# Kernel tuning notes

Hardware: AMD Instinct MI355X
Metric: run time of the kernel (lower is better)

## Reference

```python
import jax, jax.numpy as jnp
import numpy as np

KERNEL_NUM = 21
SIGMA = 0.1
EXACT_SIGMA = 0.001

def _kernel_params():
    mus, sigmas = [], []
    for i in range(KERNEL_NUM):
        mu = 1.0 / (KERNEL_NUM - 1) + 2.0 * i / (KERNEL_NUM - 1) - 1.0
        sigma = SIGMA
        if mu > 1.0:
            sigma = EXACT_SIGMA
            mu = 1.0
        mus.append(mu)
        sigmas.append(sigma)
    return np.asarray(mus, np.float32), np.asarray(sigmas, np.float32)

MU, SIG = _kernel_params()  # [K], [K]

def setup_inputs() -> dict:
    key = jax.random.key(0)
    k = jax.random.split(key, 8)
    V, D, B, L, R = 50000, 128, 512, 30, 200
    emb = jax.random.normal(k[0], (V, D), dtype=jnp.float32)
    W = jax.random.normal(k[1], (1, KERNEL_NUM), dtype=jnp.float32) * 0.1
    b = jax.random.normal(k[2], (1,), dtype=jnp.float32) * 0.1
    query1 = jax.random.randint(k[3], (B, L), 0, V, dtype=jnp.int32)
    doc1 = jax.random.randint(k[4], (B, R), 0, V, dtype=jnp.int32)
    query2 = jax.random.randint(k[5], (B, L), 0, V, dtype=jnp.int32)
    doc2 = jax.random.randint(k[6], (B, R), 0, V, dtype=jnp.int32)
    return {"emb": emb, "W": W, "b": b, "query1": query1, "doc1": doc1,
            "query2": query2, "doc2": doc2}

def _l2norm(x):
    # F.normalize(p=2, dim=-1): x / max(||x||, eps)
    n = jnp.sqrt(jnp.sum(x * x, axis=-1, keepdims=True))
    return x / jnp.maximum(n, 1e-12)

def _predict(emb, W, b, q, d):
    eq = _l2norm(emb[q])              # [B,L,D]
    ed = _l2norm(emb[d])              # [B,R,D]
    M = jnp.einsum('bld,brd->blr', eq, ed)  # matching matrix [B,L,R]
    # multi-Gaussian kernel bank: [B,L,R,K]
    Kmat = jnp.exp(-0.5 * (M[..., None] - MU) ** 2 / (SIG ** 2))
    km = jnp.sum(jnp.log1p(jnp.sum(Kmat, axis=2)), axis=1)  # [B,K]
    return km @ W.T + b               # [B,1]

def reference(emb, W, b, query1, doc1, query2, doc2):
    logits1 = _predict(emb, W, b, query1, doc1)
    logits2 = _predict(emb, W, b, query2, doc2)
    return jax.nn.sigmoid(logits1 - logits2)
```

## Files before the change

### kernel.cpp

```cpp
#include <hip/hip_runtime.h>
#include <hip/hip_fp16.h>
#include <math.h>

#define V   50000
#define DIM 128
#define BB  512
#define LQ  30
#define RD  200
#define KN  21

typedef __attribute__((ext_vector_type(8))) _Float16 f16x8;
typedef __attribute__((ext_vector_type(4))) float f32x4;
typedef __attribute__((ext_vector_type(2))) float f32x2;

#if __has_builtin(__builtin_amdgcn_exp2f)
#define EXP2F(x) __builtin_amdgcn_exp2f(x)
#else
#define EXP2F(x) __expf((x) * 0.69314718f)
#endif

#define ALPHA 72.1347520f
#define E10   22026.4657948f

static __device__ __forceinline__ f16x8 as_hfrag(int4 v) {
    return __builtin_bit_cast(f16x8, v);
}
static __device__ __forceinline__ unsigned pk2h(float a, float b) {
    return __builtin_bit_cast(unsigned, __builtin_amdgcn_cvt_pkrtz(a, b));
}
static __device__ __forceinline__ unsigned hscale(unsigned u, __half2 s) {
    return __builtin_bit_cast(unsigned, __hmul2(__builtin_bit_cast(__half2, u), s));
}

static __device__ __forceinline__ void gather_row_f16(const float* __restrict__ rowp,
                                                      int g, int4* f) {
    float ss = 0.0f;
#pragma unroll
    for (int ks = 0; ks < 4; ++ks) {
        const float4* p = reinterpret_cast<const float4*>(rowp + ks * 32 + g * 8);
        float4 a = p[0], b = p[1];
        ss = fmaf(a.x, a.x, fmaf(a.y, a.y, fmaf(a.z, a.z, fmaf(a.w, a.w, ss))));
        ss = fmaf(b.x, b.x, fmaf(b.y, b.y, fmaf(b.z, b.z, fmaf(b.w, b.w, ss))));
        f[ks].x = (int)pk2h(a.x, a.y);
        f[ks].y = (int)pk2h(a.z, a.w);
        f[ks].z = (int)pk2h(b.x, b.y);
        f[ks].w = (int)pk2h(b.z, b.w);
    }
    ss += __shfl_xor(ss, 16);
    ss += __shfl_xor(ss, 32);
    const float inv = rsqrtf(fmaxf(ss, 1e-24f));
    const __half2 h2 = __float2half2_rn(inv);
#pragma unroll
    for (int ks = 0; ks < 4; ++ks) {
        f[ks].x = (int)hscale((unsigned)f[ks].x, h2);
        f[ks].y = (int)hscale((unsigned)f[ks].y, h2);
        f[ks].z = (int)hscale((unsigned)f[ks].z, h2);
        f[ks].w = (int)hscale((unsigned)f[ks].w, h2);
    }
}

static __device__ __forceinline__ void bank4_pk(f32x4 pv, int4 dt, int qt,
                                                f32x2* ks2, float& cnt) {
    const float mv[4] = {pv[0], pv[1], pv[2], pv[3]};
    const int   dv[4] = {dt.x, dt.y, dt.z, dt.w};
    f32x2 t[4], u[4];
#pragma unroll
    for (int i = 0; i < 4; ++i) {
        float m  = mv[i];
        float dA = m + 0.5f, dB = m - 0.5f;
        float tA = EXP2F(-ALPHA * dA * (dA + 0.9f));
        float tB = EXP2F(-ALPHA * dB * (dB + 0.9f));
        float uB = EXP2F(14.4269504f * dB);
        float uA = uB * E10;
        t[i] = f32x2{tA, tB};
        u[i] = f32x2{uA, uB};
        cnt += (dv[i] == qt) ? 1.0f : 0.0f;
    }
#pragma unroll
    for (int k = 0; k < 10; ++k) {
        ks2[k] += (t[0] + t[1]) + (t[2] + t[3]);
        t[0] *= u[0]; t[1] *= u[1]; t[2] *= u[2]; t[3] *= u[3];
    }
}

__global__ __launch_bounds__(256, 4) void knrm_main(
    const float* __restrict__ emb, const float* __restrict__ W,
    const int* __restrict__ q1, const int* __restrict__ d1,
    const int* __restrict__ q2, const int* __restrict__ d2,
    float* __restrict__ logits)
{
    __shared__ int sQtok[32];
    __shared__ __align__(16) int sDtok[256];
    __shared__ float kred[4][32][KN];

    const int pb = blockIdx.x;
    const int pair = pb >> 9, b = pb & 511;
    const int* qind = (pair ? q2 : q1) + b * LQ;
    const int* dind = (pair ? d2 : d1) + b * RD;

    const int tid = threadIdx.x;
    const int lane = tid & 63, w = tid >> 6;
    const int r = lane & 15, g = lane >> 4;

    if (tid < 32) sQtok[tid] = (tid < LQ) ? qind[tid] : -2;
    { int c = tid; sDtok[c] = (c < RD) ? dind[c] : -1; }

    const int qiA = qind[r];
    const int qiB = qind[(16 + r) < LQ ? (16 + r) : LQ - 1];
    int4 qa[4], qb[4];
    gather_row_f16(emb + (size_t)qiA * DIM, g, qa);
    gather_row_f16(emb + (size_t)qiB * DIM, g, qb);

    __syncthreads();

    const int qt0 = sQtok[r], qt1 = sQtok[16 + r];
    const int4* sDtok4 = (const int4*)sDtok;

    f32x2 ks0[10], ks1[10];
#pragma unroll
    for (int k = 0; k < 10; ++k) { ks0[k] = f32x2{0.f, 0.f}; ks1[k] = f32x2{0.f, 0.f}; }
    float cnt0 = 0.0f, cnt1 = 0.0f;

    const int ns = (w < 3) ? 4 : 1;
#pragma unroll 2
    for (int s = 0; s < ns; ++s) {
        const int sbase = w * 64 + s * 16;
        const int dcol = sbase + r;
        const int di = sDtok[dcol < RD ? dcol : RD - 1];

        int4 df[4];
        gather_row_f16(emb + (size_t)di * DIM, g, df);

        f32x4 acc0 = {0.f, 0.f, 0.f, 0.f}, acc1 = {0.f, 0.f, 0.f, 0.f};
#pragma unroll
        for (int ks = 0; ks < 4; ++ks) {
            f16x8 fd = as_hfrag(df[ks]);
            acc0 = __builtin_amdgcn_mfma_f32_16x16x32_f16(fd, as_hfrag(qa[ks]), acc0, 0, 0, 0);
            acc1 = __builtin_amdgcn_mfma_f32_16x16x32_f16(fd, as_hfrag(qb[ks]), acc1, 0, 0, 0);
        }

        if (sbase + g * 4 < RD) {
            const int4 dt = sDtok4[(sbase >> 2) + g];
            bank4_pk(acc0, dt, qt0, ks0, cnt0);
            bank4_pk(acc1, dt, qt1, ks1, cnt1);
        }
    }

#pragma unroll
    for (int k = 0; k < 10; ++k) {
        float a0 = ks0[k].x, b0 = ks0[k].y, a1 = ks1[k].x, b1 = ks1[k].y;
        a0 += __shfl_xor(a0, 16); a0 += __shfl_xor(a0, 32);
        b0 += __shfl_xor(b0, 16); b0 += __shfl_xor(b0, 32);
        a1 += __shfl_xor(a1, 16); a1 += __shfl_xor(a1, 32);
        b1 += __shfl_xor(b1, 16); b1 += __shfl_xor(b1, 32);
        ks0[k] = f32x2{a0, b0};
        ks1[k] = f32x2{a1, b1};
    }
    cnt0 += __shfl_xor(cnt0, 16); cnt0 += __shfl_xor(cnt0, 32);
    cnt1 += __shfl_xor(cnt1, 16); cnt1 += __shfl_xor(cnt1, 32);

    if (lane < 16) {
        float* k0 = &kred[w][r][0];
        float* k1 = &kred[w][16 + r][0];
#pragma unroll
        for (int k = 0; k < 10; ++k) {
            k0[k] = ks0[k].x;  k0[10 + k] = ks0[k].y;
            k1[k] = ks1[k].x;  k1[10 + k] = ks1[k].y;
        }
        k0[20] = cnt0;
        k1[20] = cnt1;
    }
    __syncthreads();

    if (tid < 64) {
        float part = 0.0f;
        if (tid < LQ) {
#pragma unroll
            for (int k = 0; k < KN; ++k) {
                float s = kred[0][tid][k] + kred[1][tid][k]
                        + kred[2][tid][k] + kred[3][tid][k];
                float sc = 1.0f;
                if (k < 20) {
                    float j = (float)((k < 10) ? k : k - 10) - 4.5f;
                    sc = EXP2F(-0.721347520f * j * j);
                }
                part += W[k] * log1pf(sc * s);
            }
        }
        part += __shfl_xor(part, 1);
        part += __shfl_xor(part, 2);
        part += __shfl_xor(part, 4);
        part += __shfl_xor(part, 8);
        part += __shfl_xor(part, 16);
        part += __shfl_xor(part, 32);
        if (tid == 0) logits[pair * BB + b] = part;
    }
}

__global__ void knrm_final(const float* __restrict__ logits, float* __restrict__ out) {
    int i = blockIdx.x * blockDim.x + threadIdx.x;
    if (i < BB) {
        float x = logits[i] - logits[BB + i];
        out[i] = 1.0f / (1.0f + expf(-x));
    }
}

extern "C" void kernel_launch(void* const* d_in, const int* in_sizes, int n_in,
                              void* d_out, int out_size, void* d_ws, size_t ws_size,
                              hipStream_t stream) {
    const float* emb = (const float*)d_in[0];
    const float* W   = (const float*)d_in[1];
    const int* q1    = (const int*)d_in[3];
    const int* dd1   = (const int*)d_in[4];
    const int* q2    = (const int*)d_in[5];
    const int* dd2   = (const int*)d_in[6];

    float* logits = (float*)d_ws;

    knrm_main<<<1024, 256, 0, stream>>>(emb, W, q1, dd1, q2, dd2, logits);
    knrm_final<<<2, 256, 0, stream>>>(logits, (float*)d_out);
}
```

Baseline: 38.23 us.

## Stage normalized query rows in shared memory once per block

Each of the four waves previously gathered and normalized both query rows on its own, so every query embedding was loaded four times per block. Now all 256 threads cooperatively load the 30 query rows once, normalize them, convert to f16 and store them in an XOR-swizzled shared array, and each wave reads its MFMA fragments from there. The strip loop is also restructured with a lambda and a fixed trip count per wave, and the doc-token padding now clamps to a valid index. This adds 8 KB of LDS and a barrier before compute, which may affect occupancy and overlap of query loads with the doc gather.

```diff
diff --git a/kernel.cpp b/kernel.cpp
--- a/kernel.cpp
+++ b/kernel.cpp
@@ -91,6 +91,7 @@
 {
     __shared__ int sQtok[32];
     __shared__ __align__(16) int sDtok[256];
+    __shared__ int4 sQ[32][16];
     __shared__ float kred[4][32][KN];
 
     const int pb = blockIdx.x;
@@ -103,16 +104,43 @@
     const int r = lane & 15, g = lane >> 4;
 
     if (tid < 32) sQtok[tid] = (tid < LQ) ? qind[tid] : -2;
-    { int c = tid; sDtok[c] = (c < RD) ? dind[c] : -1; }
-
-    const int qiA = qind[r];
-    const int qiB = qind[(16 + r) < LQ ? (16 + r) : LQ - 1];
+    sDtok[tid] = dind[tid < RD ? tid : RD - 1];
+
+    {
+        const int row = tid >> 3, seg = tid & 7;
+        const int qi = qind[row < LQ ? row : LQ - 1];
+        const float4* p = reinterpret_cast<const float4*>(emb + (size_t)qi * DIM + seg * 16);
+        float4 v0 = p[0], v1 = p[1], v2 = p[2], v3 = p[3];
+        float ss = 0.0f;
+        ss = fmaf(v0.x, v0.x, fmaf(v0.y, v0.y, fmaf(v0.z, v0.z, fmaf(v0.w, v0.w, ss))));
+        ss = fmaf(v1.x, v1.x, fmaf(v1.y, v1.y, fmaf(v1.z, v1.z, fmaf(v1.w, v1.w, ss))));
+        ss = fmaf(v2.x, v2.x, fmaf(v2.y, v2.y, fmaf(v2.z, v2.z, fmaf(v2.w, v2.w, ss))));
+        ss = fmaf(v3.x, v3.x, fmaf(v3.y, v3.y, fmaf(v3.z, v3.z, fmaf(v3.w, v3.w, ss))));
+        ss += __shfl_xor(ss, 1);
+        ss += __shfl_xor(ss, 2);
+        ss += __shfl_xor(ss, 4);
+        const float inv = rsqrtf(fmaxf(ss, 1e-24f));
+        int4 s0, s1;
+        s0.x = (int)pk2h(v0.x * inv, v0.y * inv);
+        s0.y = (int)pk2h(v0.z * inv, v0.w * inv);
+        s0.z = (int)pk2h(v1.x * inv, v1.y * inv);
+        s0.w = (int)pk2h(v1.z * inv, v1.w * inv);
+        s1.x = (int)pk2h(v2.x * inv, v2.y * inv);
+        s1.y = (int)pk2h(v2.z * inv, v2.w * inv);
+        s1.z = (int)pk2h(v3.x * inv, v3.y * inv);
+        s1.w = (int)pk2h(v3.z * inv, v3.w * inv);
+        const int rw = row & 15;
+        sQ[row][(2 * seg) ^ rw]     = s0;
+        sQ[row][(2 * seg + 1) ^ rw] = s1;
+    }
+    __syncthreads();
+
     int4 qa[4], qb[4];
-    gather_row_f16(emb + (size_t)qiA * DIM, g, qa);
-    gather_row_f16(emb + (size_t)qiB * DIM, g, qb);
-
-    __syncthreads();
-
+#pragma unroll
+    for (int ks = 0; ks < 4; ++ks) {
+        qa[ks] = sQ[r][(ks * 4 + g) ^ r];
+        qb[ks] = sQ[16 + r][(ks * 4 + g) ^ r];
+    }
     const int qt0 = sQtok[r], qt1 = sQtok[16 + r];
     const int4* sDtok4 = (const int4*)sDtok;
 
@@ -121,16 +149,10 @@
     for (int k = 0; k < 10; ++k) { ks0[k] = f32x2{0.f, 0.f}; ks1[k] = f32x2{0.f, 0.f}; }
     float cnt0 = 0.0f, cnt1 = 0.0f;
 
-    const int ns = (w < 3) ? 4 : 1;
-#pragma unroll 2
-    for (int s = 0; s < ns; ++s) {
-        const int sbase = w * 64 + s * 16;
-        const int dcol = sbase + r;
-        const int di = sDtok[dcol < RD ? dcol : RD - 1];
-
+    auto strip = [&](int sbase) {
+        const int di = sDtok[sbase + r];
         int4 df[4];
         gather_row_f16(emb + (size_t)di * DIM, g, df);
-
         f32x4 acc0 = {0.f, 0.f, 0.f, 0.f}, acc1 = {0.f, 0.f, 0.f, 0.f};
 #pragma unroll
         for (int ks = 0; ks < 4; ++ks) {
@@ -138,12 +160,18 @@
             acc0 = __builtin_amdgcn_mfma_f32_16x16x32_f16(fd, as_hfrag(qa[ks]), acc0, 0, 0, 0);
             acc1 = __builtin_amdgcn_mfma_f32_16x16x32_f16(fd, as_hfrag(qb[ks]), acc1, 0, 0, 0);
         }
-
         if (sbase + g * 4 < RD) {
             const int4 dt = sDtok4[(sbase >> 2) + g];
             bank4_pk(acc0, dt, qt0, ks0, cnt0);
             bank4_pk(acc1, dt, qt1, ks1, cnt1);
         }
+    };
+
+    if (w < 3) {
+#pragma unroll 2
+        for (int s = 0; s < 4; ++s) strip(w * 64 + s * 16);
+    } else {
+        strip(192);
     }
 
 #pragma unroll
```

Measured after the change: 33.98 us. 11.1% less time.

## Prefetch doc rows one strip ahead and stage normalized queries in LDS

Applied to the files above, without the earlier changes.

Doc embedding row loads are split into issue and pack phases so the next strip's global loads are in flight while the current strip runs MFMA and the kernel bank. Strips are interleaved across waves (w, w+4, w+8, plus a tail strip on wave 0) instead of each wave taking a contiguous block, which balances work across the four waves. Query rows are loaded cooperatively once per block, normalized in fp32, and stored in a swizzled LDS array rather than held in registers by every wave. The prefetch buffer raises register pressure, and query fragments are now read from LDS inside the inner loop.

```diff
diff --git a/kernel.cpp b/kernel.cpp
--- a/kernel.cpp
+++ b/kernel.cpp
@@ -32,20 +32,46 @@
     return __builtin_bit_cast(unsigned, __hmul2(__builtin_bit_cast(__half2, u), s));
 }
 
-static __device__ __forceinline__ void gather_row_f16(const float* __restrict__ rowp,
-                                                      int g, int4* f) {
-    float ss = 0.0f;
+static __device__ __forceinline__ void issue_row_loads(const float* __restrict__ rowp,
+                                                       int g, float4* raw) {
 #pragma unroll
     for (int ks = 0; ks < 4; ++ks) {
         const float4* p = reinterpret_cast<const float4*>(rowp + ks * 32 + g * 8);
-        float4 a = p[0], b = p[1];
-        ss = fmaf(a.x, a.x, fmaf(a.y, a.y, fmaf(a.z, a.z, fmaf(a.w, a.w, ss))));
-        ss = fmaf(b.x, b.x, fmaf(b.y, b.y, fmaf(b.z, b.z, fmaf(b.w, b.w, ss))));
-        f[ks].x = (int)pk2h(a.x, a.y);
-        f[ks].y = (int)pk2h(a.z, a.w);
-        f[ks].z = (int)pk2h(b.x, b.y);
-        f[ks].w = (int)pk2h(b.z, b.w);
-    }
+        raw[2 * ks]     = p[0];
+        raw[2 * ks + 1] = p[1];
+    }
+}
+static __device__ __forceinline__ void pack_row(const float4* raw, int4* f) {
+    float c0 = 0.f, c1 = 0.f, c2 = 0.f, c3 = 0.f;
+    {
+        float4 a = raw[0], b = raw[1];
+        c0 = fmaf(a.x, a.x, fmaf(a.y, a.y, c0)); c1 = fmaf(a.z, a.z, fmaf(a.w, a.w, c1));
+        c2 = fmaf(b.x, b.x, fmaf(b.y, b.y, c2)); c3 = fmaf(b.z, b.z, fmaf(b.w, b.w, c3));
+        f[0].x = (int)pk2h(a.x, a.y); f[0].y = (int)pk2h(a.z, a.w);
+        f[0].z = (int)pk2h(b.x, b.y); f[0].w = (int)pk2h(b.z, b.w);
+    }
+    {
+        float4 a = raw[2], b = raw[3];
+        c0 = fmaf(a.x, a.x, fmaf(a.y, a.y, c0)); c1 = fmaf(a.z, a.z, fmaf(a.w, a.w, c1));
+        c2 = fmaf(b.x, b.x, fmaf(b.y, b.y, c2)); c3 = fmaf(b.z, b.z, fmaf(b.w, b.w, c3));
+        f[1].x = (int)pk2h(a.x, a.y); f[1].y = (int)pk2h(a.z, a.w);
+        f[1].z = (int)pk2h(b.x, b.y); f[1].w = (int)pk2h(b.z, b.w);
+    }
+    {
+        float4 a = raw[4], b = raw[5];
+        c0 = fmaf(a.x, a.x, fmaf(a.y, a.y, c0)); c1 = fmaf(a.z, a.z, fmaf(a.w, a.w, c1));
+        c2 = fmaf(b.x, b.x, fmaf(b.y, b.y, c2)); c3 = fmaf(b.z, b.z, fmaf(b.w, b.w, c3));
+        f[2].x = (int)pk2h(a.x, a.y); f[2].y = (int)pk2h(a.z, a.w);
+        f[2].z = (int)pk2h(b.x, b.y); f[2].w = (int)pk2h(b.z, b.w);
+    }
+    {
+        float4 a = raw[6], b = raw[7];
+        c0 = fmaf(a.x, a.x, fmaf(a.y, a.y, c0)); c1 = fmaf(a.z, a.z, fmaf(a.w, a.w, c1));
+        c2 = fmaf(b.x, b.x, fmaf(b.y, b.y, c2)); c3 = fmaf(b.z, b.z, fmaf(b.w, b.w, c3));
+        f[3].x = (int)pk2h(a.x, a.y); f[3].y = (int)pk2h(a.z, a.w);
+        f[3].z = (int)pk2h(b.x, b.y); f[3].w = (int)pk2h(b.z, b.w);
+    }
+    float ss = (c0 + c1) + (c2 + c3);
     ss += __shfl_xor(ss, 16);
     ss += __shfl_xor(ss, 32);
     const float inv = rsqrtf(fmaxf(ss, 1e-24f));
@@ -91,6 +117,7 @@
 {
     __shared__ int sQtok[32];
     __shared__ __align__(16) int sDtok[256];
+    __shared__ int4 sQ[32][16];
     __shared__ float kred[4][32][KN];
 
     const int pb = blockIdx.x;
@@ -103,14 +130,36 @@
     const int r = lane & 15, g = lane >> 4;
 
     if (tid < 32) sQtok[tid] = (tid < LQ) ? qind[tid] : -2;
-    { int c = tid; sDtok[c] = (c < RD) ? dind[c] : -1; }
-
-    const int qiA = qind[r];
-    const int qiB = qind[(16 + r) < LQ ? (16 + r) : LQ - 1];
-    int4 qa[4], qb[4];
-    gather_row_f16(emb + (size_t)qiA * DIM, g, qa);
-    gather_row_f16(emb + (size_t)qiB * DIM, g, qb);
-
+    sDtok[tid] = dind[tid < RD ? tid : RD - 1];
+
+    {
+        const int row = tid >> 3, seg = tid & 7;
+        const int qi = qind[row < LQ ? row : LQ - 1];
+        const float4* p = reinterpret_cast<const float4*>(emb + (size_t)qi * DIM + seg * 16);
+        float4 v0 = p[0], v1 = p[1], v2 = p[2], v3 = p[3];
+        float s0 = 0.f, s1 = 0.f, s2 = 0.f, s3 = 0.f;
+        s0 = fmaf(v0.x, v0.x, fmaf(v0.y, v0.y, s0)); s1 = fmaf(v0.z, v0.z, fmaf(v0.w, v0.w, s1));
+        s2 = fmaf(v1.x, v1.x, fmaf(v1.y, v1.y, s2)); s3 = fmaf(v1.z, v1.z, fmaf(v1.w, v1.w, s3));
+        s0 = fmaf(v2.x, v2.x, fmaf(v2.y, v2.y, s0)); s1 = fmaf(v2.z, v2.z, fmaf(v2.w, v2.w, s1));
+        s2 = fmaf(v3.x, v3.x, fmaf(v3.y, v3.y, s2)); s3 = fmaf(v3.z, v3.z, fmaf(v3.w, v3.w, s3));
+        float ss = (s0 + s1) + (s2 + s3);
+        ss += __shfl_xor(ss, 1);
+        ss += __shfl_xor(ss, 2);
+        ss += __shfl_xor(ss, 4);
+        const float inv = rsqrtf(fmaxf(ss, 1e-24f));
+        int4 t0, t1;
+        t0.x = (int)pk2h(v0.x * inv, v0.y * inv);
+        t0.y = (int)pk2h(v0.z * inv, v0.w * inv);
+        t0.z = (int)pk2h(v1.x * inv, v1.y * inv);
+        t0.w = (int)pk2h(v1.z * inv, v1.w * inv);
+        t1.x = (int)pk2h(v2.x * inv, v2.y * inv);
+        t1.y = (int)pk2h(v2.z * inv, v2.w * inv);
+        t1.z = (int)pk2h(v3.x * inv, v3.y * inv);
+        t1.w = (int)pk2h(v3.z * inv, v3.w * inv);
+        const int rw = row & 15;
+        sQ[row][(2 * seg) ^ rw]     = t0;
+        sQ[row][(2 * seg + 1) ^ rw] = t1;
+    }
     __syncthreads();
 
     const int qt0 = sQtok[r], qt1 = sQtok[16 + r];
@@ -121,28 +170,44 @@
     for (int k = 0; k < 10; ++k) { ks0[k] = f32x2{0.f, 0.f}; ks1[k] = f32x2{0.f, 0.f}; }
     float cnt0 = 0.0f, cnt1 = 0.0f;
 
-    const int ns = (w < 3) ? 4 : 1;
-#pragma unroll 2
-    for (int s = 0; s < ns; ++s) {
-        const int sbase = w * 64 + s * 16;
-        const int dcol = sbase + r;
-        const int di = sDtok[dcol < RD ? dcol : RD - 1];
-
-        int4 df[4];
-        gather_row_f16(emb + (size_t)di * DIM, g, df);
-
+    auto do_strip = [&](const int4* df, int sbase) {
         f32x4 acc0 = {0.f, 0.f, 0.f, 0.f}, acc1 = {0.f, 0.f, 0.f, 0.f};
 #pragma unroll
         for (int ks = 0; ks < 4; ++ks) {
             f16x8 fd = as_hfrag(df[ks]);
-            acc0 = __builtin_amdgcn_mfma_f32_16x16x32_f16(fd, as_hfrag(qa[ks]), acc0, 0, 0, 0);
-            acc1 = __builtin_amdgcn_mfma_f32_16x16x32_f16(fd, as_hfrag(qb[ks]), acc1, 0, 0, 0);
-        }
-
+            acc0 = __builtin_amdgcn_mfma_f32_16x16x32_f16(fd, as_hfrag(sQ[r][(ks * 4 + g) ^ r]), acc0, 0, 0, 0);
+            acc1 = __builtin_amdgcn_mfma_f32_16x16x32_f16(fd, as_hfrag(sQ[16 + r][(ks * 4 + g) ^ r]), acc1, 0, 0, 0);
+        }
         if (sbase + g * 4 < RD) {
             const int4 dt = sDtok4[(sbase >> 2) + g];
             bank4_pk(acc0, dt, qt0, ks0, cnt0);
             bank4_pk(acc1, dt, qt1, ks1, cnt1);
+        }
+    };
+
+    {
+        float4 raw[8];
+        int4 df[4];
+        const int sb0 = w * 16, sb1 = (w + 4) * 16, sb2 = (w + 8) * 16;
+
+        issue_row_loads(emb + (size_t)sDtok[sb0 + r] * DIM, g, raw);
+
+        pack_row(raw, df);
+        issue_row_loads(emb + (size_t)sDtok[sb1 + r] * DIM, g, raw);
+        do_strip(df, sb0);
+
+        pack_row(raw, df);
+        issue_row_loads(emb + (size_t)sDtok[sb2 + r] * DIM, g, raw);
+        do_strip(df, sb1);
+
+        pack_row(raw, df);
+        if (w == 0)
+            issue_row_loads(emb + (size_t)sDtok[192 + r] * DIM, g, raw);
+        do_strip(df, sb2);
+
+        if (w == 0) {
+            pack_row(raw, df);
+            do_strip(df, 192);
         }
     }
 
```

Measured after the change: 53.54 us. 40.0% more time.

## Stage normalized query rows in shared memory and software-pipeline doc row gathers

Applied to the files above, without the earlier changes.

The block now gathers and normalizes the 30 query rows cooperatively, one row per 8 threads, and stores them as f16 in an XOR-swizzled shared-memory tile. This replaces each wave separately loading two query rows into registers. The doc-strip loop is unrolled by hand so the embedding loads for the next strip are issued before the MFMA and Gaussian-bank work on the current strip, hiding gather latency. Strips are interleaved across waves (w*16 + 64*s), so each wave handles three strips and wave 0 takes the tail strip, instead of three waves doing four and one doing one. In exchange, the prefetched float4 registers raise register pressure and the MFMA operands now come through shared-memory reads.

```diff
diff --git a/kernel.cpp b/kernel.cpp
--- a/kernel.cpp
+++ b/kernel.cpp
@@ -30,33 +30,6 @@
 }
 static __device__ __forceinline__ unsigned hscale(unsigned u, __half2 s) {
     return __builtin_bit_cast(unsigned, __hmul2(__builtin_bit_cast(__half2, u), s));
-}
-
-static __device__ __forceinline__ void gather_row_f16(const float* __restrict__ rowp,
-                                                      int g, int4* f) {
-    float ss = 0.0f;
-#pragma unroll
-    for (int ks = 0; ks < 4; ++ks) {
-        const float4* p = reinterpret_cast<const float4*>(rowp + ks * 32 + g * 8);
-        float4 a = p[0], b = p[1];
-        ss = fmaf(a.x, a.x, fmaf(a.y, a.y, fmaf(a.z, a.z, fmaf(a.w, a.w, ss))));
-        ss = fmaf(b.x, b.x, fmaf(b.y, b.y, fmaf(b.z, b.z, fmaf(b.w, b.w, ss))));
-        f[ks].x = (int)pk2h(a.x, a.y);
-        f[ks].y = (int)pk2h(a.z, a.w);
-        f[ks].z = (int)pk2h(b.x, b.y);
-        f[ks].w = (int)pk2h(b.z, b.w);
-    }
-    ss += __shfl_xor(ss, 16);
-    ss += __shfl_xor(ss, 32);
-    const float inv = rsqrtf(fmaxf(ss, 1e-24f));
-    const __half2 h2 = __float2half2_rn(inv);
-#pragma unroll
-    for (int ks = 0; ks < 4; ++ks) {
-        f[ks].x = (int)hscale((unsigned)f[ks].x, h2);
-        f[ks].y = (int)hscale((unsigned)f[ks].y, h2);
-        f[ks].z = (int)hscale((unsigned)f[ks].z, h2);
-        f[ks].w = (int)hscale((unsigned)f[ks].w, h2);
-    }
 }
 
 static __device__ __forceinline__ void bank4_pk(f32x4 pv, int4 dt, int qt,
@@ -83,6 +56,59 @@
     }
 }
 
+#define LOADROW(sb) do {                                                      \
+    const float* rp_ = emb + (size_t)sDtok[(sb) + r] * DIM + g * 8;           \
+    r0 = *(const float4*)(rp_);        r1 = *(const float4*)(rp_ + 4);        \
+    r2 = *(const float4*)(rp_ + 32);   r3 = *(const float4*)(rp_ + 36);       \
+    r4 = *(const float4*)(rp_ + 64);   r5 = *(const float4*)(rp_ + 68);       \
+    r6 = *(const float4*)(rp_ + 96);   r7 = *(const float4*)(rp_ + 100);      \
+} while (0)
+
+#define PACKROW() do {                                                        \
+    float c0_, c1_, c2_, c3_;                                                 \
+    c0_ = fmaf(r0.x,r0.x,fmaf(r0.y,r0.y,0.f)); c1_ = fmaf(r0.z,r0.z,fmaf(r0.w,r0.w,0.f)); \
+    c2_ = fmaf(r1.x,r1.x,fmaf(r1.y,r1.y,0.f)); c3_ = fmaf(r1.z,r1.z,fmaf(r1.w,r1.w,0.f)); \
+    c0_ = fmaf(r2.x,r2.x,fmaf(r2.y,r2.y,c0_)); c1_ = fmaf(r2.z,r2.z,fmaf(r2.w,r2.w,c1_)); \
+    c2_ = fmaf(r3.x,r3.x,fmaf(r3.y,r3.y,c2_)); c3_ = fmaf(r3.z,r3.z,fmaf(r3.w,r3.w,c3_)); \
+    c0_ = fmaf(r4.x,r4.x,fmaf(r4.y,r4.y,c0_)); c1_ = fmaf(r4.z,r4.z,fmaf(r4.w,r4.w,c1_)); \
+    c2_ = fmaf(r5.x,r5.x,fmaf(r5.y,r5.y,c2_)); c3_ = fmaf(r5.z,r5.z,fmaf(r5.w,r5.w,c3_)); \
+    c0_ = fmaf(r6.x,r6.x,fmaf(r6.y,r6.y,c0_)); c1_ = fmaf(r6.z,r6.z,fmaf(r6.w,r6.w,c1_)); \
+    c2_ = fmaf(r7.x,r7.x,fmaf(r7.y,r7.y,c2_)); c3_ = fmaf(r7.z,r7.z,fmaf(r7.w,r7.w,c3_)); \
+    float ss_ = (c0_ + c1_) + (c2_ + c3_);                                    \
+    ss_ += __shfl_xor(ss_, 16);  ss_ += __shfl_xor(ss_, 32);                  \
+    const float inv_ = rsqrtf(fmaxf(ss_, 1e-24f));                            \
+    const __half2 h2_ = __float2half2_rn(inv_);                               \
+    d0.x = (int)hscale(pk2h(r0.x, r0.y), h2_); d0.y = (int)hscale(pk2h(r0.z, r0.w), h2_); \
+    d0.z = (int)hscale(pk2h(r1.x, r1.y), h2_); d0.w = (int)hscale(pk2h(r1.z, r1.w), h2_); \
+    d1.x = (int)hscale(pk2h(r2.x, r2.y), h2_); d1.y = (int)hscale(pk2h(r2.z, r2.w), h2_); \
+    d1.z = (int)hscale(pk2h(r3.x, r3.y), h2_); d1.w = (int)hscale(pk2h(r3.z, r3.w), h2_); \
+    d2.x = (int)hscale(pk2h(r4.x, r4.y), h2_); d2.y = (int)hscale(pk2h(r4.z, r4.w), h2_); \
+    d2.z = (int)hscale(pk2h(r5.x, r5.y), h2_); d2.w = (int)hscale(pk2h(r5.z, r5.w), h2_); \
+    d3.x = (int)hscale(pk2h(r6.x, r6.y), h2_); d3.y = (int)hscale(pk2h(r6.z, r6.w), h2_); \
+    d3.z = (int)hscale(pk2h(r7.x, r7.y), h2_); d3.w = (int)hscale(pk2h(r7.z, r7.w), h2_); \
+} while (0)
+
+#define DOSTRIP(sb) do {                                                      \
+    f32x4 acc0_ = {0.f,0.f,0.f,0.f}, acc1_ = {0.f,0.f,0.f,0.f};               \
+    { f16x8 fd_ = as_hfrag(d0);                                               \
+      acc0_ = __builtin_amdgcn_mfma_f32_16x16x32_f16(fd_, as_hfrag(sQ[r][(0+g)^r]), acc0_,0,0,0);      \
+      acc1_ = __builtin_amdgcn_mfma_f32_16x16x32_f16(fd_, as_hfrag(sQ[16+r][(0+g)^r]), acc1_,0,0,0); } \
+    { f16x8 fd_ = as_hfrag(d1);                                               \
+      acc0_ = __builtin_amdgcn_mfma_f32_16x16x32_f16(fd_, as_hfrag(sQ[r][(4+g)^r]), acc0_,0,0,0);      \
+      acc1_ = __builtin_amdgcn_mfma_f32_16x16x32_f16(fd_, as_hfrag(sQ[16+r][(4+g)^r]), acc1_,0,0,0); } \
+    { f16x8 fd_ = as_hfrag(d2);                                               \
+      acc0_ = __builtin_amdgcn_mfma_f32_16x16x32_f16(fd_, as_hfrag(sQ[r][(8+g)^r]), acc0_,0,0,0);      \
+      acc1_ = __builtin_amdgcn_mfma_f32_16x16x32_f16(fd_, as_hfrag(sQ[16+r][(8+g)^r]), acc1_,0,0,0); } \
+    { f16x8 fd_ = as_hfrag(d3);                                               \
+      acc0_ = __builtin_amdgcn_mfma_f32_16x16x32_f16(fd_, as_hfrag(sQ[r][(12+g)^r]), acc0_,0,0,0);     \
+      acc1_ = __builtin_amdgcn_mfma_f32_16x16x32_f16(fd_, as_hfrag(sQ[16+r][(12+g)^r]), acc1_,0,0,0); }\
+    if ((sb) + g * 4 < RD) {                                                  \
+        const int4 dt_ = sDtok4[((sb) >> 2) + g];                             \
+        bank4_pk(acc0_, dt_, qt0, ks0, cnt0);                                 \
+        bank4_pk(acc1_, dt_, qt1, ks1, cnt1);                                 \
+    }                                                                         \
+} while (0)
+
 __global__ __launch_bounds__(256, 4) void knrm_main(
     const float* __restrict__ emb, const float* __restrict__ W,
     const int* __restrict__ q1, const int* __restrict__ d1,
@@ -91,6 +117,7 @@
 {
     __shared__ int sQtok[32];
     __shared__ __align__(16) int sDtok[256];
+    __shared__ int4 sQ[32][16];
     __shared__ float kred[4][32][KN];
 
     const int pb = blockIdx.x;
@@ -103,14 +130,37 @@
     const int r = lane & 15, g = lane >> 4;
 
     if (tid < 32) sQtok[tid] = (tid < LQ) ? qind[tid] : -2;
-    { int c = tid; sDtok[c] = (c < RD) ? dind[c] : -1; }
-
-    const int qiA = qind[r];
-    const int qiB = qind[(16 + r) < LQ ? (16 + r) : LQ - 1];
-    int4 qa[4], qb[4];
-    gather_row_f16(emb + (size_t)qiA * DIM, g, qa);
-    gather_row_f16(emb + (size_t)qiB * DIM, g, qb);
-
+    sDtok[tid] = dind[tid < RD ? tid : RD - 1];
+
+    {
+        const int row = tid >> 3, seg = tid & 7;
+        const int qi = qind[row < LQ ? row : LQ - 1];
+        const float4* p = reinterpret_cast<const float4*>(emb + (size_t)qi * DIM + seg * 16);
+        float4 v0 = p[0], v1 = p[1], v2 = p[2], v3 = p[3];
+        float s0 = 0.f, s1 = 0.f, s2 = 0.f, s3 = 0.f;
+        s0 = fmaf(v0.x, v0.x, fmaf(v0.y, v0.y, s0)); s1 = fmaf(v0.z, v0.z, fmaf(v0.w, v0.w, s1));
+        s2 = fmaf(v1.x, v1.x, fmaf(v1.y, v1.y, s2)); s3 = fmaf(v1.z, v1.z, fmaf(v1.w, v1.w, s3));
+        s0 = fmaf(v2.x, v2.x, fmaf(v2.y, v2.y, s0)); s1 = fmaf(v2.z, v2.z, fmaf(v2.w, v2.w, s1));
+        s2 = fmaf(v3.x, v3.x, fmaf(v3.y, v3.y, s2)); s3 = fmaf(v3.z, v3.z, fmaf(v3.w, v3.w, s3));
+        float ss = (s0 + s1) + (s2 + s3);
+        ss += __shfl_xor(ss, 1);
+        ss += __shfl_xor(ss, 2);
+        ss += __shfl_xor(ss, 4);
+        const float inv = rsqrtf(fmaxf(ss, 1e-24f));
+        const __half2 h2 = __float2half2_rn(inv);
+        int4 t0, t1;
+        t0.x = (int)hscale(pk2h(v0.x, v0.y), h2);
+        t0.y = (int)hscale(pk2h(v0.z, v0.w), h2);
+        t0.z = (int)hscale(pk2h(v1.x, v1.y), h2);
+        t0.w = (int)hscale(pk2h(v1.z, v1.w), h2);
+        t1.x = (int)hscale(pk2h(v2.x, v2.y), h2);
+        t1.y = (int)hscale(pk2h(v2.z, v2.w), h2);
+        t1.z = (int)hscale(pk2h(v3.x, v3.y), h2);
+        t1.w = (int)hscale(pk2h(v3.z, v3.w), h2);
+        const int rw = row & 15;
+        sQ[row][(2 * seg) ^ rw]     = t0;
+        sQ[row][(2 * seg + 1) ^ rw] = t1;
+    }
     __syncthreads();
 
     const int qt0 = sQtok[r], qt1 = sQtok[16 + r];
@@ -121,28 +171,24 @@
     for (int k = 0; k < 10; ++k) { ks0[k] = f32x2{0.f, 0.f}; ks1[k] = f32x2{0.f, 0.f}; }
     float cnt0 = 0.0f, cnt1 = 0.0f;
 
-    const int ns = (w < 3) ? 4 : 1;
-#pragma unroll 2
-    for (int s = 0; s < ns; ++s) {
-        const int sbase = w * 64 + s * 16;
-        const int dcol = sbase + r;
-        const int di = sDtok[dcol < RD ? dcol : RD - 1];
-
-        int4 df[4];
-        gather_row_f16(emb + (size_t)di * DIM, g, df);
-
-        f32x4 acc0 = {0.f, 0.f, 0.f, 0.f}, acc1 = {0.f, 0.f, 0.f, 0.f};
-#pragma unroll
-        for (int ks = 0; ks < 4; ++ks) {
-            f16x8 fd = as_hfrag(df[ks]);
-            acc0 = __builtin_amdgcn_mfma_f32_16x16x32_f16(fd, as_hfrag(qa[ks]), acc0, 0, 0, 0);
-            acc1 = __builtin_amdgcn_mfma_f32_16x16x32_f16(fd, as_hfrag(qb[ks]), acc1, 0, 0, 0);
-        }
-
-        if (sbase + g * 4 < RD) {
-            const int4 dt = sDtok4[(sbase >> 2) + g];
-            bank4_pk(acc0, dt, qt0, ks0, cnt0);
-            bank4_pk(acc1, dt, qt1, ks1, cnt1);
+    {
+        float4 r0, r1, r2, r3, r4, r5, r6, r7;
+        int4 d0, d1, d2, d3;
+        const int sb0 = w * 16, sb1 = sb0 + 64, sb2 = sb0 + 128;
+
+        LOADROW(sb0);
+        PACKROW();
+        LOADROW(sb1);
+        DOSTRIP(sb0);
+        PACKROW();
+        LOADROW(sb2);
+        DOSTRIP(sb1);
+        PACKROW();
+        if (w == 0) LOADROW(192);
+        DOSTRIP(sb2);
+        if (w == 0) {
+            PACKROW();
+            DOSTRIP(192);
         }
     }
 
```

Result: slower. 51.43 us (+34.5%).
